# Kernel tuning notes

Hardware: AMD Instinct MI355X
Metric: run time of the kernel (lower is better)

Reference implementation:

```python
import jax, jax.numpy as jnp
import numpy as np

B, C, H, W = 32, 64, 128, 128


def setup_inputs() -> dict:
    key = jax.random.key(0)
    ks = jax.random.split(key, 9)
    s = 1.0 / np.sqrt(C)
    return {
        "q": jax.random.normal(ks[0], (B, C, H, W), dtype=jnp.float32),
        "k": jax.random.normal(ks[1], (B, C, H, W), dtype=jnp.float32),
        "v": jax.random.normal(ks[2], (B, C, H, W), dtype=jnp.float32),
        "wq": jax.random.normal(ks[3], (C, C), dtype=jnp.float32) * s,
        "bq": jax.random.normal(ks[4], (C,), dtype=jnp.float32) * s,
        "wk": jax.random.normal(ks[5], (C, C), dtype=jnp.float32) * s,
        "bk": jax.random.normal(ks[6], (C,), dtype=jnp.float32) * s,
        "wv": jax.random.normal(ks[7], (C, C), dtype=jnp.float32) * s,
        "bv": jax.random.normal(ks[8], (C,), dtype=jnp.float32) * s,
    }


def reference(q, k, v, wq, bq, wk, bk, wv, bv):
    # 1x1 conv == per-pixel linear over channels; fuse permute(0,2,3,1) into einsum
    qp = jnp.einsum('bchw,oc->bhwo', q, wq) + bq  # [B,H,W,C]
    kp = jnp.einsum('bchw,oc->bhwo', k, wk) + bk  # [B,H,W,C]
    vp = jnp.einsum('bchw,oc->bhwo', v, wv) + bv  # [B,H,W,C]
    # unnormalized attention along W axis, batched over (B, H)
    attn = jnp.einsum('bhwc,bhxc->bhwx', qp, kp)   # [B,H,W,W]
    out = jnp.einsum('bhwx,bhxc->bhwc', attn, vp)  # [B,H,W,C]
    return jnp.transpose(out, (0, 3, 1, 2)) + q    # back to [B,C,H,W] + residual
```

## Files before the change

### kernel.cpp

```cpp
#include <hip/hip_runtime.h>
#include <hip/hip_bf16.h>


typedef __bf16 bf16x8 __attribute__((ext_vector_type(8)));
typedef float  f32x4  __attribute__((ext_vector_type(4)));

#define LDP 68
#define LDX 132

#define OF_A 0
#define OF_B 8704
#define OF_C 17408
#define OF_D 25856
#define OF_W 34304
#define OF_SB 38656
#define LDS_USHORTS (38656 + 384)

__device__ __forceinline__ unsigned short f2bf(float x) {
  __hip_bfloat16 h = __float2bfloat16(x);
  return __builtin_bit_cast(unsigned short, h);
}
__device__ __forceinline__ float bf2f(unsigned short u) {
  unsigned int t = ((unsigned int)u) << 16;
  return __builtin_bit_cast(float, t);
}
__device__ __forceinline__ unsigned int pack2(float a, float b) {
  return (unsigned int)f2bf(a) | ((unsigned int)f2bf(b) << 16);
}
__device__ __forceinline__ bf16x8 cvt8(float4 a, float4 b) {
  union { unsigned int u[4]; bf16x8 v; } r;
  r.u[0] = pack2(a.x, a.y); r.u[1] = pack2(a.z, a.w);
  r.u[2] = pack2(b.x, b.y); r.u[3] = pack2(b.z, b.w);
  return r.v;
}
__device__ __forceinline__ bf16x8 ld8(const unsigned short* p) {
  uint2 lo = *reinterpret_cast<const uint2*>(p);
  uint2 hi = *reinterpret_cast<const uint2*>(p + 4);
  uint4 t;
  t.x = lo.x; t.y = lo.y; t.z = hi.x; t.w = hi.y;
  return __builtin_bit_cast(bf16x8, t);
}

__global__ __launch_bounds__(512, 4)
void fused_mha(const float* __restrict__ q, const float* __restrict__ k,
               const float* __restrict__ v,
               const float* __restrict__ wq, const float* __restrict__ bq,
               const float* __restrict__ wk, const float* __restrict__ bk,
               const float* __restrict__ wv, const float* __restrict__ bv,
               float* __restrict__ out)
{
  __shared__ __align__(16) unsigned short lds[LDS_USHORTS];
  unsigned short* sK   = lds + OF_A;
  unsigned short* sV   = lds + OF_B;
  unsigned short* sKPt = lds + OF_C;
  unsigned short* sVPt = lds + OF_D;
  unsigned short* sWq  = lds + OF_W;
  unsigned short* sTt  = lds + OF_A;
  unsigned short* sQ   = lds + OF_B;
  unsigned short* sQP  = lds + OF_C;
  float* sB = (float*)(lds + OF_SB);

  const int tid  = threadIdx.x;
  const int lane = tid & 63;
  const int ww   = tid >> 6;
  const int l15  = lane & 15;
  const int g    = lane >> 4;

  const int bh = blockIdx.x;
  const int bi = bh >> 7;
  const int hi = bh & 127;
  const size_t CS   = 128*128;
  const size_t base = (size_t)bi * (64*CS) + (size_t)hi * 128;

  const int sw0 = 4*(tid & 31);
  const int scA = 2*((tid >> 5) & 15);

  const int rt = ww & 3;
  const int cb = (ww >> 2) * 4;
  bf16x8 wkf[2], wvf[2];
  #pragma unroll
  for (int ks = 0; ks < 2; ++ks) {
    const float* pk = wk + (16*rt + l15)*64 + 8*g + 32*ks;
    const float* pv = wv + (16*rt + l15)*64 + 8*g + 32*ks;
    wkf[ks] = cvt8(*(const float4*)pk, *(const float4*)(pk+4));
    wvf[ks] = cvt8(*(const float4*)pv, *(const float4*)(pv+4));
  }
  float4 qreg[4];
  #pragma unroll
  for (int u = 0; u < 2; ++u) {
    int c = scA + 32*u;
    qreg[2*u+0] = *(const float4*)(q + base + (size_t)c    *CS + sw0);
    qreg[2*u+1] = *(const float4*)(q + base + (size_t)(c+1)*CS + sw0);
  }
  #pragma unroll
  for (int u = 0; u < 2; ++u) {
    int c = scA + 32*u;
    float4 ka = *(const float4*)(k + base + (size_t)c    *CS + sw0);
    float4 kb = *(const float4*)(k + base + (size_t)(c+1)*CS + sw0);
    float4 va = *(const float4*)(v + base + (size_t)c    *CS + sw0);
    float4 vb = *(const float4*)(v + base + (size_t)(c+1)*CS + sw0);
    const float* kaf = (const float*)&ka; const float* kbf = (const float*)&kb;
    const float* vaf = (const float*)&va; const float* vbf = (const float*)&vb;
    #pragma unroll
    for (int j = 0; j < 4; ++j) {
      *(unsigned int*)&sK[(sw0+j)*LDP + c] = pack2(kaf[j], kbf[j]);
      *(unsigned int*)&sV[(sw0+j)*LDP + c] = pack2(vaf[j], vbf[j]);
    }
  }
  {
    const int o  = tid >> 3;
    const int c0 = (tid & 7) * 8;
    float4 a = *(const float4*)(wq + o*64 + c0);
    float4 b = *(const float4*)(wq + o*64 + c0 + 4);
    unsigned short* p = &sWq[o*LDP + c0];
    ((uint2*)p)[0] = make_uint2(pack2(a.x,a.y), pack2(a.z,a.w));
    ((uint2*)p)[1] = make_uint2(pack2(b.x,b.y), pack2(b.z,b.w));
  }
  if (tid < 64)        sB[tid]       = bq[tid];
  else if (tid < 128)  sB[tid]       = bk[tid-64];
  else if (tid < 192)  sB[tid]       = bv[tid-128];
  __syncthreads();

  {
    f32x4 z = {0.f,0.f,0.f,0.f};
    f32x4 acck[4] = {z,z,z,z}, accv[4] = {z,z,z,z};
    #pragma unroll
    for (int ks = 0; ks < 2; ++ks) {
      #pragma unroll
      for (int cc = 0; cc < 4; ++cc) {
        bf16x8 bk8 = ld8(&sK[(16*(cb+cc) + l15)*LDP + 32*ks + 8*g]);
        bf16x8 bv8 = ld8(&sV[(16*(cb+cc) + l15)*LDP + 32*ks + 8*g]);
        acck[cc] = __builtin_amdgcn_mfma_f32_16x16x32_bf16(wkf[ks], bk8, acck[cc], 0, 0, 0);
        accv[cc] = __builtin_amdgcn_mfma_f32_16x16x32_bf16(wvf[ks], bv8, accv[cc], 0, 0, 0);
      }
    }
    #pragma unroll
    for (int cc = 0; cc < 4; ++cc) {
      int x = 16*(cb+cc) + l15;
      #pragma unroll
      for (int r = 0; r < 4; ++r) {
        int o = 16*rt + 4*g + r;
        sKPt[o*LDX + x] = f2bf(acck[cc][r] + sB[64 + o]);
        sVPt[o*LDX + x] = f2bf(accv[cc][r] + sB[128 + o]);
      }
    }
  }
  __syncthreads();

  {
    const int rt2 = ww >> 1;
    const int cb2 = (ww & 1) * 2;
    f32x4 z = {0.f,0.f,0.f,0.f};
    f32x4 acc[2] = {z,z};
    #pragma unroll
    for (int ks = 0; ks < 4; ++ks) {
      bf16x8 a = ld8(&sVPt[(16*rt2 + l15)*LDX + 32*ks + 8*g]);
      #pragma unroll
      for (int cc = 0; cc < 2; ++cc) {
        bf16x8 b = ld8(&sKPt[(16*(cb2+cc) + l15)*LDX + 32*ks + 8*g]);
        acc[cc] = __builtin_amdgcn_mfma_f32_16x16x32_bf16(a, b, acc[cc], 0, 0, 0);
      }
    }
    #pragma unroll
    for (int u = 0; u < 2; ++u) {
      int c = scA + 32*u;
      const float* qa = (const float*)&qreg[2*u];
      const float* qb = (const float*)&qreg[2*u+1];
      #pragma unroll
      for (int j = 0; j < 4; ++j)
        *(unsigned int*)&sQ[(sw0+j)*LDP + c] = pack2(qa[j], qb[j]);
    }
    #pragma unroll
    for (int cc = 0; cc < 2; ++cc) {
      int d = 16*(cb2+cc) + l15;
      #pragma unroll
      for (int r = 0; r < 4; ++r)
        sTt[(16*rt2 + 4*g + r)*LDP + d] = f2bf(acc[cc][r]);
    }
  }
  __syncthreads();

  {
    f32x4 z = {0.f,0.f,0.f,0.f};
    f32x4 acc[4] = {z,z,z,z};
    #pragma unroll
    for (int ks = 0; ks < 2; ++ks) {
      bf16x8 a = ld8(&sQ[(16*ww + l15)*LDP + 32*ks + 8*g]);
      #pragma unroll
      for (int ct = 0; ct < 4; ++ct) {
        bf16x8 b = ld8(&sWq[(16*ct + l15)*LDP + 32*ks + 8*g]);
        acc[ct] = __builtin_amdgcn_mfma_f32_16x16x32_bf16(a, b, acc[ct], 0, 0, 0);
      }
    }
    #pragma unroll
    for (int ct = 0; ct < 4; ++ct) {
      float bias = sB[16*ct + l15];
      #pragma unroll
      for (int r = 0; r < 4; ++r)
        sQP[(16*ww + 4*g + r)*LDP + 16*ct + l15] = f2bf(acc[ct][r] + bias);
    }
  }
  __syncthreads();

  {
    f32x4 z = {0.f,0.f,0.f,0.f};
    f32x4 acc[4] = {z,z,z,z};
    #pragma unroll
    for (int ks = 0; ks < 2; ++ks) {
      bf16x8 a = ld8(&sQP[(16*ww + l15)*LDP + 32*ks + 8*g]);
      #pragma unroll
      for (int ct = 0; ct < 4; ++ct) {
        bf16x8 b = ld8(&sTt[(16*ct + l15)*LDP + 32*ks + 8*g]);
        acc[ct] = __builtin_amdgcn_mfma_f32_16x16x32_bf16(a, b, acc[ct], 0, 0, 0);
      }
    }
    #pragma unroll
    for (int ct = 0; ct < 4; ++ct) {
      int c  = 16*ct + l15;
      int w0 = 16*ww + 4*g;
      float4 o4;
      o4.x = acc[ct][0] + bf2f(sQ[(w0+0)*LDP + c]);
      o4.y = acc[ct][1] + bf2f(sQ[(w0+1)*LDP + c]);
      o4.z = acc[ct][2] + bf2f(sQ[(w0+2)*LDP + c]);
      o4.w = acc[ct][3] + bf2f(sQ[(w0+3)*LDP + c]);
      *reinterpret_cast<float4*>(out + base + (size_t)c * CS + w0) = o4;
    }
  }
}

extern "C" void kernel_launch(void* const* d_in, const int* in_sizes, int n_in,
                              void* d_out, int out_size, void* d_ws, size_t ws_size,
                              hipStream_t stream) {
  (void)in_sizes; (void)n_in; (void)d_ws; (void)ws_size; (void)out_size;
  const float* q  = (const float*)d_in[0];
  const float* k  = (const float*)d_in[1];
  const float* v  = (const float*)d_in[2];
  const float* wq = (const float*)d_in[3];
  const float* bq = (const float*)d_in[4];
  const float* wk = (const float*)d_in[5];
  const float* bk = (const float*)d_in[6];
  const float* wv = (const float*)d_in[7];
  const float* bv = (const float*)d_in[8];
  float* out = (float*)d_out;
  fused_mha<<<dim3(32*128), dim3(512), 0, stream>>>(q, k, v, wq, bq, wk, bk, wv, bv, out);
}
```

Baseline: 112.6 us.

## Make blocks loop over eight rows with register prefetch and swizzled LDS

Each block now processes eight consecutive (batch,row) slices in a loop instead of one, prefetching the next slice's q/k/v into registers while the current slice's matmuls run. An XOR swizzle is applied to the sK/sV/sQ LDS tiles to reduce bank conflicts on the transposed stores, and one intra-wave barrier is removed. The grid shrinks to 512 blocks, which lowers resident waves per CU and relies on the software prefetch to hide global-memory latency.

```diff
diff --git a/kernel.cpp b/kernel.cpp
--- a/kernel.cpp
+++ b/kernel.cpp
@@ -15,6 +15,8 @@
 #define OF_W 34304
 #define OF_SB 38656
 #define LDS_USHORTS (38656 + 384)
+
+#define SWZ(row, col) ((col) ^ ((((row) >> 2) & 7) << 3))
 
 __device__ __forceinline__ unsigned short f2bf(float x) {
   __hip_bfloat16 h = __float2bfloat16(x);
@@ -66,14 +68,11 @@
   const int l15  = lane & 15;
   const int g    = lane >> 4;
 
-  const int bh = blockIdx.x;
-  const int bi = bh >> 7;
-  const int hi = bh & 127;
-  const size_t CS   = 128*128;
-  const size_t base = (size_t)bi * (64*CS) + (size_t)hi * 128;
-
-  const int sw0 = 4*(tid & 31);
-  const int scA = 2*((tid >> 5) & 15);
+  const size_t CS = 128*128;
+
+  const int sw0   = 4*(tid & 31);
+  const int scA   = 2*((tid >> 5) & 15);
+  const int swsel = ((tid & 31) & 7) << 3;
 
   const int rt = ww & 3;
   const int cb = (ww >> 2) * 4;
@@ -85,28 +84,6 @@
     wkf[ks] = cvt8(*(const float4*)pk, *(const float4*)(pk+4));
     wvf[ks] = cvt8(*(const float4*)pv, *(const float4*)(pv+4));
   }
-  float4 qreg[4];
-  #pragma unroll
-  for (int u = 0; u < 2; ++u) {
-    int c = scA + 32*u;
-    qreg[2*u+0] = *(const float4*)(q + base + (size_t)c    *CS + sw0);
-    qreg[2*u+1] = *(const float4*)(q + base + (size_t)(c+1)*CS + sw0);
-  }
-  #pragma unroll
-  for (int u = 0; u < 2; ++u) {
-    int c = scA + 32*u;
-    float4 ka = *(const float4*)(k + base + (size_t)c    *CS + sw0);
-    float4 kb = *(const float4*)(k + base + (size_t)(c+1)*CS + sw0);
-    float4 va = *(const float4*)(v + base + (size_t)c    *CS + sw0);
-    float4 vb = *(const float4*)(v + base + (size_t)(c+1)*CS + sw0);
-    const float* kaf = (const float*)&ka; const float* kbf = (const float*)&kb;
-    const float* vaf = (const float*)&va; const float* vbf = (const float*)&vb;
-    #pragma unroll
-    for (int j = 0; j < 4; ++j) {
-      *(unsigned int*)&sK[(sw0+j)*LDP + c] = pack2(kaf[j], kbf[j]);
-      *(unsigned int*)&sV[(sw0+j)*LDP + c] = pack2(vaf[j], vbf[j]);
-    }
-  }
   {
     const int o  = tid >> 3;
     const int c0 = (tid & 7) * 8;
@@ -116,115 +93,176 @@
     ((uint2*)p)[0] = make_uint2(pack2(a.x,a.y), pack2(a.z,a.w));
     ((uint2*)p)[1] = make_uint2(pack2(b.x,b.y), pack2(b.z,b.w));
   }
-  if (tid < 64)        sB[tid]       = bq[tid];
-  else if (tid < 128)  sB[tid]       = bk[tid-64];
-  else if (tid < 192)  sB[tid]       = bv[tid-128];
-  __syncthreads();
-
+  if (tid < 64)        sB[tid] = bq[tid];
+  else if (tid < 128)  sB[tid] = bk[tid-64];
+  else if (tid < 192)  sB[tid] = bv[tid-128];
+
+  float4 qreg[4], kreg[4], vreg[4];
   {
-    f32x4 z = {0.f,0.f,0.f,0.f};
-    f32x4 acck[4] = {z,z,z,z}, accv[4] = {z,z,z,z};
-    #pragma unroll
-    for (int ks = 0; ks < 2; ++ks) {
-      #pragma unroll
-      for (int cc = 0; cc < 4; ++cc) {
-        bf16x8 bk8 = ld8(&sK[(16*(cb+cc) + l15)*LDP + 32*ks + 8*g]);
-        bf16x8 bv8 = ld8(&sV[(16*(cb+cc) + l15)*LDP + 32*ks + 8*g]);
-        acck[cc] = __builtin_amdgcn_mfma_f32_16x16x32_bf16(wkf[ks], bk8, acck[cc], 0, 0, 0);
-        accv[cc] = __builtin_amdgcn_mfma_f32_16x16x32_bf16(wvf[ks], bv8, accv[cc], 0, 0, 0);
-      }
-    }
-    #pragma unroll
-    for (int cc = 0; cc < 4; ++cc) {
-      int x = 16*(cb+cc) + l15;
-      #pragma unroll
-      for (int r = 0; r < 4; ++r) {
-        int o = 16*rt + 4*g + r;
-        sKPt[o*LDX + x] = f2bf(acck[cc][r] + sB[64 + o]);
-        sVPt[o*LDX + x] = f2bf(accv[cc][r] + sB[128 + o]);
-      }
-    }
-  }
-  __syncthreads();
-
-  {
-    const int rt2 = ww >> 1;
-    const int cb2 = (ww & 1) * 2;
-    f32x4 z = {0.f,0.f,0.f,0.f};
-    f32x4 acc[2] = {z,z};
-    #pragma unroll
-    for (int ks = 0; ks < 4; ++ks) {
-      bf16x8 a = ld8(&sVPt[(16*rt2 + l15)*LDX + 32*ks + 8*g]);
-      #pragma unroll
-      for (int cc = 0; cc < 2; ++cc) {
-        bf16x8 b = ld8(&sKPt[(16*(cb2+cc) + l15)*LDX + 32*ks + 8*g]);
-        acc[cc] = __builtin_amdgcn_mfma_f32_16x16x32_bf16(a, b, acc[cc], 0, 0, 0);
-      }
-    }
+    const int bh = blockIdx.x << 3;
+    const size_t b0 = (size_t)(bh >> 7)*(64*CS) + (size_t)(bh & 127)*128;
     #pragma unroll
     for (int u = 0; u < 2; ++u) {
       int c = scA + 32*u;
-      const float* qa = (const float*)&qreg[2*u];
-      const float* qb = (const float*)&qreg[2*u+1];
-      #pragma unroll
-      for (int j = 0; j < 4; ++j)
-        *(unsigned int*)&sQ[(sw0+j)*LDP + c] = pack2(qa[j], qb[j]);
-    }
+      const float* pq = q + b0 + (size_t)c*CS + sw0;
+      const float* pk = k + b0 + (size_t)c*CS + sw0;
+      const float* pv = v + b0 + (size_t)c*CS + sw0;
+      qreg[2*u+0] = *(const float4*)pq;  qreg[2*u+1] = *(const float4*)(pq + CS);
+      kreg[2*u+0] = *(const float4*)pk;  kreg[2*u+1] = *(const float4*)(pk + CS);
+      vreg[2*u+0] = *(const float4*)pv;  vreg[2*u+1] = *(const float4*)(pv + CS);
+    }
+  }
+
+  for (int t = 0; t < 8; ++t) {
+    const int bh = (blockIdx.x << 3) + t;
+    const size_t base = (size_t)(bh >> 7)*(64*CS) + (size_t)(bh & 127)*128;
+    size_t nbase = 0;
+    if (t < 7) {
+      const int nbh = bh + 1;
+      nbase = (size_t)(nbh >> 7)*(64*CS) + (size_t)(nbh & 127)*128;
+    }
+
     #pragma unroll
-    for (int cc = 0; cc < 2; ++cc) {
-      int d = 16*(cb2+cc) + l15;
-      #pragma unroll
-      for (int r = 0; r < 4; ++r)
-        sTt[(16*rt2 + 4*g + r)*LDP + d] = f2bf(acc[cc][r]);
-    }
-  }
-  __syncthreads();
-
-  {
-    f32x4 z = {0.f,0.f,0.f,0.f};
-    f32x4 acc[4] = {z,z,z,z};
-    #pragma unroll
-    for (int ks = 0; ks < 2; ++ks) {
-      bf16x8 a = ld8(&sQ[(16*ww + l15)*LDP + 32*ks + 8*g]);
+    for (int u = 0; u < 2; ++u) {
+      int c = (scA + 32*u) ^ swsel;
+      const float* ka = (const float*)&kreg[2*u];
+      const float* kb = (const float*)&kreg[2*u+1];
+      const float* va = (const float*)&vreg[2*u];
+      const float* vb = (const float*)&vreg[2*u+1];
+      #pragma unroll
+      for (int j = 0; j < 4; ++j) {
+        *(unsigned int*)&sK[(sw0+j)*LDP + c] = pack2(ka[j], kb[j]);
+        *(unsigned int*)&sV[(sw0+j)*LDP + c] = pack2(va[j], vb[j]);
+      }
+    }
+    __syncthreads();
+
+    {
+      f32x4 z = {0.f,0.f,0.f,0.f};
+      f32x4 acck[4] = {z,z,z,z}, accv[4] = {z,z,z,z};
+      #pragma unroll
+      for (int ks = 0; ks < 2; ++ks) {
+        #pragma unroll
+        for (int cc = 0; cc < 4; ++cc) {
+          int row = 16*(cb+cc) + l15;
+          int col = SWZ(row, 32*ks + 8*g);
+          bf16x8 bk8 = ld8(&sK[row*LDP + col]);
+          bf16x8 bv8 = ld8(&sV[row*LDP + col]);
+          acck[cc] = __builtin_amdgcn_mfma_f32_16x16x32_bf16(wkf[ks], bk8, acck[cc], 0, 0, 0);
+          accv[cc] = __builtin_amdgcn_mfma_f32_16x16x32_bf16(wvf[ks], bv8, accv[cc], 0, 0, 0);
+        }
+      }
+      #pragma unroll
+      for (int cc = 0; cc < 4; ++cc) {
+        int x = 16*(cb+cc) + l15;
+        #pragma unroll
+        for (int r = 0; r < 4; ++r) {
+          int o = 16*rt + 4*g + r;
+          sKPt[o*LDX + x] = f2bf(acck[cc][r] + sB[64 + o]);
+          sVPt[o*LDX + x] = f2bf(accv[cc][r] + sB[128 + o]);
+        }
+      }
+    }
+    __syncthreads();
+
+    if (t < 7) {
+      #pragma unroll
+      for (int u = 0; u < 2; ++u) {
+        int c = scA + 32*u;
+        const float* pk = k + nbase + (size_t)c*CS + sw0;
+        const float* pv = v + nbase + (size_t)c*CS + sw0;
+        kreg[2*u+0] = *(const float4*)pk;  kreg[2*u+1] = *(const float4*)(pk + CS);
+        vreg[2*u+0] = *(const float4*)pv;  vreg[2*u+1] = *(const float4*)(pv + CS);
+      }
+    }
+    {
+      const int rt2 = ww >> 1;
+      const int cb2 = (ww & 1) * 2;
+      f32x4 z = {0.f,0.f,0.f,0.f};
+      f32x4 acc[2] = {z,z};
+      #pragma unroll
+      for (int ks = 0; ks < 4; ++ks) {
+        bf16x8 a = ld8(&sVPt[(16*rt2 + l15)*LDX + 32*ks + 8*g]);
+        #pragma unroll
+        for (int cc = 0; cc < 2; ++cc) {
+          bf16x8 b = ld8(&sKPt[(16*(cb2+cc) + l15)*LDX + 32*ks + 8*g]);
+          acc[cc] = __builtin_amdgcn_mfma_f32_16x16x32_bf16(a, b, acc[cc], 0, 0, 0);
+        }
+      }
+      #pragma unroll
+      for (int u = 0; u < 2; ++u) {
+        int c = (scA + 32*u) ^ swsel;
+        const float* qa = (const float*)&qreg[2*u];
+        const float* qb = (const float*)&qreg[2*u+1];
+        #pragma unroll
+        for (int j = 0; j < 4; ++j)
+          *(unsigned int*)&sQ[(sw0+j)*LDP + c] = pack2(qa[j], qb[j]);
+      }
+      #pragma unroll
+      for (int cc = 0; cc < 2; ++cc) {
+        int d = 16*(cb2+cc) + l15;
+        #pragma unroll
+        for (int r = 0; r < 4; ++r)
+          sTt[(16*rt2 + 4*g + r)*LDP + d] = f2bf(acc[cc][r]);
+      }
+    }
+    __syncthreads();
+
+    if (t < 7) {
+      #pragma unroll
+      for (int u = 0; u < 2; ++u) {
+        int c = scA + 32*u;
+        const float* pq = q + nbase + (size_t)c*CS + sw0;
+        qreg[2*u+0] = *(const float4*)pq;  qreg[2*u+1] = *(const float4*)(pq + CS);
+      }
+    }
+    {
+      f32x4 z = {0.f,0.f,0.f,0.f};
+      f32x4 acc[4] = {z,z,z,z};
+      #pragma unroll
+      for (int ks = 0; ks < 2; ++ks) {
+        int row = 16*ww + l15;
+        bf16x8 a = ld8(&sQ[row*LDP + SWZ(row, 32*ks + 8*g)]);
+        #pragma unroll
+        for (int ct = 0; ct < 4; ++ct) {
+          bf16x8 b = ld8(&sWq[(16*ct + l15)*LDP + 32*ks + 8*g]);
+          acc[ct] = __builtin_amdgcn_mfma_f32_16x16x32_bf16(a, b, acc[ct], 0, 0, 0);
+        }
+      }
       #pragma unroll
       for (int ct = 0; ct < 4; ++ct) {
-        bf16x8 b = ld8(&sWq[(16*ct + l15)*LDP + 32*ks + 8*g]);
-        acc[ct] = __builtin_amdgcn_mfma_f32_16x16x32_bf16(a, b, acc[ct], 0, 0, 0);
-      }
-    }
-    #pragma unroll
-    for (int ct = 0; ct < 4; ++ct) {
-      float bias = sB[16*ct + l15];
-      #pragma unroll
-      for (int r = 0; r < 4; ++r)
-        sQP[(16*ww + 4*g + r)*LDP + 16*ct + l15] = f2bf(acc[ct][r] + bias);
-    }
-  }
-  __syncthreads();
-
-  {
-    f32x4 z = {0.f,0.f,0.f,0.f};
-    f32x4 acc[4] = {z,z,z,z};
-    #pragma unroll
-    for (int ks = 0; ks < 2; ++ks) {
-      bf16x8 a = ld8(&sQP[(16*ww + l15)*LDP + 32*ks + 8*g]);
+        float bias = sB[16*ct + l15];
+        #pragma unroll
+        for (int r = 0; r < 4; ++r)
+          sQP[(16*ww + 4*g + r)*LDP + 16*ct + l15] = f2bf(acc[ct][r] + bias);
+      }
+    }
+
+    {
+      f32x4 z = {0.f,0.f,0.f,0.f};
+      f32x4 acc[4] = {z,z,z,z};
+      #pragma unroll
+      for (int ks = 0; ks < 2; ++ks) {
+        bf16x8 a = ld8(&sQP[(16*ww + l15)*LDP + 32*ks + 8*g]);
+        #pragma unroll
+        for (int ct = 0; ct < 4; ++ct) {
+          bf16x8 b = ld8(&sTt[(16*ct + l15)*LDP + 32*ks + 8*g]);
+          acc[ct] = __builtin_amdgcn_mfma_f32_16x16x32_bf16(a, b, acc[ct], 0, 0, 0);
+        }
+      }
       #pragma unroll
       for (int ct = 0; ct < 4; ++ct) {
-        bf16x8 b = ld8(&sTt[(16*ct + l15)*LDP + 32*ks + 8*g]);
-        acc[ct] = __builtin_amdgcn_mfma_f32_16x16x32_bf16(a, b, acc[ct], 0, 0, 0);
-      }
-    }
-    #pragma unroll
-    for (int ct = 0; ct < 4; ++ct) {
-      int c  = 16*ct + l15;
-      int w0 = 16*ww + 4*g;
-      float4 o4;
-      o4.x = acc[ct][0] + bf2f(sQ[(w0+0)*LDP + c]);
-      o4.y = acc[ct][1] + bf2f(sQ[(w0+1)*LDP + c]);
-      o4.z = acc[ct][2] + bf2f(sQ[(w0+2)*LDP + c]);
-      o4.w = acc[ct][3] + bf2f(sQ[(w0+3)*LDP + c]);
-      *reinterpret_cast<float4*>(out + base + (size_t)c * CS + w0) = o4;
-    }
+        int c  = 16*ct + l15;
+        int w0 = 16*ww + 4*g;
+        float4 o4;
+        o4.x = acc[ct][0] + bf2f(sQ[(w0+0)*LDP + SWZ(w0+0, c)]);
+        o4.y = acc[ct][1] + bf2f(sQ[(w0+1)*LDP + SWZ(w0+1, c)]);
+        o4.z = acc[ct][2] + bf2f(sQ[(w0+2)*LDP + SWZ(w0+2, c)]);
+        o4.w = acc[ct][3] + bf2f(sQ[(w0+3)*LDP + SWZ(w0+3, c)]);
+        *reinterpret_cast<float4*>(out + base + (size_t)c * CS + w0) = o4;
+      }
+    }
+    __syncthreads();
   }
 }
 
@@ -242,5 +280,5 @@
   const float* wv = (const float*)d_in[7];
   const float* bv = (const float*)d_in[8];
   float* out = (float*)d_out;
-  fused_mha<<<dim3(32*128), dim3(512), 0, stream>>>(q, k, v, wq, bq, wk, bk, wv, bv, out);
-}
+  fused_mha<<<dim3(512), dim3(512), 0, stream>>>(q, k, v, wq, bq, wk, bk, wv, bv, out);
+}
```

Result: slower. 173.3 us (+53.8%).

## Halve LDS footprint by processing K/V projection in two W-halves with swizzled layout

Applied to the files above, without the earlier changes.

The K/V projection and the V^T·K product now run over two 64-column halves of the W axis, reusing half-sized LDS staging buffers. The LDS budget per block drops substantially, which should let more blocks reside per CU, and the launch-bounds hint is raised to match. An XOR swizzle is applied to the staged K/V/Q tiles to reduce bank conflicts on the transposed writes. One barrier between the Q-projection and output stages is removed because each wave only reads back its own rows. The costs are an extra barrier per half and more serialized phases, and the Q loads move later in the kernel.

```diff
diff --git a/kernel.cpp b/kernel.cpp
--- a/kernel.cpp
+++ b/kernel.cpp
@@ -6,15 +6,17 @@
 typedef float  f32x4  __attribute__((ext_vector_type(4)));
 
 #define LDP 68
-#define LDX 132
-
-#define OF_A 0
-#define OF_B 8704
-#define OF_C 17408
-#define OF_D 25856
-#define OF_W 34304
-#define OF_SB 38656
-#define LDS_USHORTS (38656 + 384)
+
+#define OF_KS 0
+#define OF_VS 4352
+#define OF_KP 8704
+#define OF_VP 13056
+#define OF_TT 17408
+#define OF_WQ 21760
+#define OF_SB 26112
+#define LDS_USHORTS (26112 + 384)
+
+#define SWZ(row, col) ((col) ^ ((((row) >> 2) & 7) << 3))
 
 __device__ __forceinline__ unsigned short f2bf(float x) {
   __hip_bfloat16 h = __float2bfloat16(x);
@@ -41,7 +43,7 @@
   return __builtin_bit_cast(bf16x8, t);
 }
 
-__global__ __launch_bounds__(512, 4)
+__global__ __launch_bounds__(512, 6)
 void fused_mha(const float* __restrict__ q, const float* __restrict__ k,
                const float* __restrict__ v,
                const float* __restrict__ wq, const float* __restrict__ bq,
@@ -50,14 +52,14 @@
                float* __restrict__ out)
 {
   __shared__ __align__(16) unsigned short lds[LDS_USHORTS];
-  unsigned short* sK   = lds + OF_A;
-  unsigned short* sV   = lds + OF_B;
-  unsigned short* sKPt = lds + OF_C;
-  unsigned short* sVPt = lds + OF_D;
-  unsigned short* sWq  = lds + OF_W;
-  unsigned short* sTt  = lds + OF_A;
-  unsigned short* sQ   = lds + OF_B;
-  unsigned short* sQP  = lds + OF_C;
+  unsigned short* sKS = lds + OF_KS;
+  unsigned short* sVS = lds + OF_VS;
+  unsigned short* sKP = lds + OF_KP;
+  unsigned short* sVP = lds + OF_VP;
+  unsigned short* sTt = lds + OF_TT;
+  unsigned short* sWq = lds + OF_WQ;
+  unsigned short* sQ  = lds + OF_KS;
+  unsigned short* sQP = lds + OF_KP;
   float* sB = (float*)(lds + OF_SB);
 
   const int tid  = threadIdx.x;
@@ -66,17 +68,24 @@
   const int l15  = lane & 15;
   const int g    = lane >> 4;
 
+  const size_t CS = 128*128;
   const int bh = blockIdx.x;
-  const int bi = bh >> 7;
-  const int hi = bh & 127;
-  const size_t CS   = 128*128;
-  const size_t base = (size_t)bi * (64*CS) + (size_t)hi * 128;
-
-  const int sw0 = 4*(tid & 31);
-  const int scA = 2*((tid >> 5) & 15);
-
+  const size_t base = (size_t)(bh >> 7)*(64*CS) + (size_t)(bh & 127)*128;
+
+  const int sw0 = 4*(tid & 15);
+  const int scA = 2*((tid >> 4) & 31);
+  const int swk = ((tid & 15) & 7) << 3;
+
+  float4 kreg[4], vreg[4];
+  #pragma unroll
+  for (int h = 0; h < 2; ++h)
+    #pragma unroll
+    for (int e = 0; e < 2; ++e) {
+      kreg[2*h+e] = *(const float4*)(k + base + (size_t)(scA+e)*CS + sw0 + 64*h);
+      vreg[2*h+e] = *(const float4*)(v + base + (size_t)(scA+e)*CS + sw0 + 64*h);
+    }
   const int rt = ww & 3;
-  const int cb = (ww >> 2) * 4;
+  const int xb = (ww >> 2) * 2;
   bf16x8 wkf[2], wvf[2];
   #pragma unroll
   for (int ks = 0; ks < 2; ++ks) {
@@ -85,28 +94,6 @@
     wkf[ks] = cvt8(*(const float4*)pk, *(const float4*)(pk+4));
     wvf[ks] = cvt8(*(const float4*)pv, *(const float4*)(pv+4));
   }
-  float4 qreg[4];
-  #pragma unroll
-  for (int u = 0; u < 2; ++u) {
-    int c = scA + 32*u;
-    qreg[2*u+0] = *(const float4*)(q + base + (size_t)c    *CS + sw0);
-    qreg[2*u+1] = *(const float4*)(q + base + (size_t)(c+1)*CS + sw0);
-  }
-  #pragma unroll
-  for (int u = 0; u < 2; ++u) {
-    int c = scA + 32*u;
-    float4 ka = *(const float4*)(k + base + (size_t)c    *CS + sw0);
-    float4 kb = *(const float4*)(k + base + (size_t)(c+1)*CS + sw0);
-    float4 va = *(const float4*)(v + base + (size_t)c    *CS + sw0);
-    float4 vb = *(const float4*)(v + base + (size_t)(c+1)*CS + sw0);
-    const float* kaf = (const float*)&ka; const float* kbf = (const float*)&kb;
-    const float* vaf = (const float*)&va; const float* vbf = (const float*)&vb;
-    #pragma unroll
-    for (int j = 0; j < 4; ++j) {
-      *(unsigned int*)&sK[(sw0+j)*LDP + c] = pack2(kaf[j], kbf[j]);
-      *(unsigned int*)&sV[(sw0+j)*LDP + c] = pack2(vaf[j], vbf[j]);
-    }
-  }
   {
     const int o  = tid >> 3;
     const int c0 = (tid & 7) * 8;
@@ -116,76 +103,117 @@
     ((uint2*)p)[0] = make_uint2(pack2(a.x,a.y), pack2(a.z,a.w));
     ((uint2*)p)[1] = make_uint2(pack2(b.x,b.y), pack2(b.z,b.w));
   }
-  if (tid < 64)        sB[tid]       = bq[tid];
-  else if (tid < 128)  sB[tid]       = bk[tid-64];
-  else if (tid < 192)  sB[tid]       = bv[tid-128];
+  if (tid < 64)        sB[tid] = bq[tid];
+  else if (tid < 128)  sB[tid] = bk[tid-64];
+  else if (tid < 192)  sB[tid] = bv[tid-128];
+
+  {
+    const int c = scA ^ swk;
+    const float* ka = (const float*)&kreg[0];
+    const float* kb = (const float*)&kreg[1];
+    const float* va = (const float*)&vreg[0];
+    const float* vb = (const float*)&vreg[1];
+    #pragma unroll
+    for (int j = 0; j < 4; ++j) {
+      *(unsigned int*)&sKS[(sw0+j)*LDP + c] = pack2(ka[j], kb[j]);
+      *(unsigned int*)&sVS[(sw0+j)*LDP + c] = pack2(va[j], vb[j]);
+    }
+  }
   __syncthreads();
 
-  {
-    f32x4 z = {0.f,0.f,0.f,0.f};
-    f32x4 acck[4] = {z,z,z,z}, accv[4] = {z,z,z,z};
+  f32x4 z = {0.f,0.f,0.f,0.f};
+  f32x4 tacc[2] = {z, z};
+  const int rt2 = ww >> 1;
+  const int cb2 = (ww & 1) * 2;
+  float4 qreg[4];
+
+  #pragma unroll
+  for (int h = 0; h < 2; ++h) {
+    {
+      f32x4 acck[2] = {z,z}, accv[2] = {z,z};
+      #pragma unroll
+      for (int ks = 0; ks < 2; ++ks) {
+        #pragma unroll
+        for (int cc = 0; cc < 2; ++cc) {
+          int row = 16*(xb+cc) + l15;
+          int col = SWZ(row, 32*ks + 8*g);
+          bf16x8 bk8 = ld8(&sKS[row*LDP + col]);
+          bf16x8 bv8 = ld8(&sVS[row*LDP + col]);
+          acck[cc] = __builtin_amdgcn_mfma_f32_16x16x32_bf16(wkf[ks], bk8, acck[cc], 0, 0, 0);
+          accv[cc] = __builtin_amdgcn_mfma_f32_16x16x32_bf16(wvf[ks], bv8, accv[cc], 0, 0, 0);
+        }
+      }
+      #pragma unroll
+      for (int cc = 0; cc < 2; ++cc) {
+        int xl = 16*(xb+cc) + l15;
+        #pragma unroll
+        for (int r = 0; r < 4; ++r) {
+          int o = 16*rt + 4*g + r;
+          sKP[o*LDP + xl] = f2bf(acck[cc][r] + sB[64 + o]);
+          sVP[o*LDP + xl] = f2bf(accv[cc][r] + sB[128 + o]);
+        }
+      }
+    }
+    __syncthreads();
+
+    if (h == 0) {
+      const int c = scA ^ swk;
+      const float* ka = (const float*)&kreg[2];
+      const float* kb = (const float*)&kreg[3];
+      const float* va = (const float*)&vreg[2];
+      const float* vb = (const float*)&vreg[3];
+      #pragma unroll
+      for (int j = 0; j < 4; ++j) {
+        *(unsigned int*)&sKS[(sw0+j)*LDP + c] = pack2(ka[j], kb[j]);
+        *(unsigned int*)&sVS[(sw0+j)*LDP + c] = pack2(va[j], vb[j]);
+      }
+      #pragma unroll
+      for (int hh = 0; hh < 2; ++hh)
+        #pragma unroll
+        for (int e = 0; e < 2; ++e)
+          qreg[2*hh+e] = *(const float4*)(q + base + (size_t)(scA+e)*CS + sw0 + 64*hh);
+    } else {
+      #pragma unroll
+      for (int hh = 0; hh < 2; ++hh) {
+        const int c = scA ^ swk;
+        const float* qa = (const float*)&qreg[2*hh];
+        const float* qb = (const float*)&qreg[2*hh+1];
+        #pragma unroll
+        for (int j = 0; j < 4; ++j)
+          *(unsigned int*)&sQ[(sw0 + 64*hh + j)*LDP + c] = pack2(qa[j], qb[j]);
+      }
+    }
+    {
+      #pragma unroll
+      for (int ks = 0; ks < 2; ++ks) {
+        int arow = 16*rt2 + l15;
+        bf16x8 a = ld8(&sVP[arow*LDP + 32*ks + 8*g]);
+        #pragma unroll
+        for (int cc = 0; cc < 2; ++cc) {
+          int brow = 16*(cb2+cc) + l15;
+          bf16x8 b = ld8(&sKP[brow*LDP + 32*ks + 8*g]);
+          tacc[cc] = __builtin_amdgcn_mfma_f32_16x16x32_bf16(a, b, tacc[cc], 0, 0, 0);
+        }
+      }
+    }
+    if (h == 1) {
+      #pragma unroll
+      for (int cc = 0; cc < 2; ++cc) {
+        int d = 16*(cb2+cc) + l15;
+        #pragma unroll
+        for (int r = 0; r < 4; ++r)
+          sTt[(16*rt2 + 4*g + r)*LDP + d] = f2bf(tacc[cc][r]);
+      }
+    }
+    __syncthreads();
+  }
+
+  {
+    f32x4 acc[4] = {z,z,z,z};
     #pragma unroll
     for (int ks = 0; ks < 2; ++ks) {
-      #pragma unroll
-      for (int cc = 0; cc < 4; ++cc) {
-        bf16x8 bk8 = ld8(&sK[(16*(cb+cc) + l15)*LDP + 32*ks + 8*g]);
-        bf16x8 bv8 = ld8(&sV[(16*(cb+cc) + l15)*LDP + 32*ks + 8*g]);
-        acck[cc] = __builtin_amdgcn_mfma_f32_16x16x32_bf16(wkf[ks], bk8, acck[cc], 0, 0, 0);
-        accv[cc] = __builtin_amdgcn_mfma_f32_16x16x32_bf16(wvf[ks], bv8, accv[cc], 0, 0, 0);
-      }
-    }
-    #pragma unroll
-    for (int cc = 0; cc < 4; ++cc) {
-      int x = 16*(cb+cc) + l15;
-      #pragma unroll
-      for (int r = 0; r < 4; ++r) {
-        int o = 16*rt + 4*g + r;
-        sKPt[o*LDX + x] = f2bf(acck[cc][r] + sB[64 + o]);
-        sVPt[o*LDX + x] = f2bf(accv[cc][r] + sB[128 + o]);
-      }
-    }
-  }
-  __syncthreads();
-
-  {
-    const int rt2 = ww >> 1;
-    const int cb2 = (ww & 1) * 2;
-    f32x4 z = {0.f,0.f,0.f,0.f};
-    f32x4 acc[2] = {z,z};
-    #pragma unroll
-    for (int ks = 0; ks < 4; ++ks) {
-      bf16x8 a = ld8(&sVPt[(16*rt2 + l15)*LDX + 32*ks + 8*g]);
-      #pragma unroll
-      for (int cc = 0; cc < 2; ++cc) {
-        bf16x8 b = ld8(&sKPt[(16*(cb2+cc) + l15)*LDX + 32*ks + 8*g]);
-        acc[cc] = __builtin_amdgcn_mfma_f32_16x16x32_bf16(a, b, acc[cc], 0, 0, 0);
-      }
-    }
-    #pragma unroll
-    for (int u = 0; u < 2; ++u) {
-      int c = scA + 32*u;
-      const float* qa = (const float*)&qreg[2*u];
-      const float* qb = (const float*)&qreg[2*u+1];
-      #pragma unroll
-      for (int j = 0; j < 4; ++j)
-        *(unsigned int*)&sQ[(sw0+j)*LDP + c] = pack2(qa[j], qb[j]);
-    }
-    #pragma unroll
-    for (int cc = 0; cc < 2; ++cc) {
-      int d = 16*(cb2+cc) + l15;
-      #pragma unroll
-      for (int r = 0; r < 4; ++r)
-        sTt[(16*rt2 + 4*g + r)*LDP + d] = f2bf(acc[cc][r]);
-    }
-  }
-  __syncthreads();
-
-  {
-    f32x4 z = {0.f,0.f,0.f,0.f};
-    f32x4 acc[4] = {z,z,z,z};
-    #pragma unroll
-    for (int ks = 0; ks < 2; ++ks) {
-      bf16x8 a = ld8(&sQ[(16*ww + l15)*LDP + 32*ks + 8*g]);
+      int arow = 16*ww + l15;
+      bf16x8 a = ld8(&sQ[arow*LDP + SWZ(arow, 32*ks + 8*g)]);
       #pragma unroll
       for (int ct = 0; ct < 4; ++ct) {
         bf16x8 b = ld8(&sWq[(16*ct + l15)*LDP + 32*ks + 8*g]);
@@ -200,10 +228,8 @@
         sQP[(16*ww + 4*g + r)*LDP + 16*ct + l15] = f2bf(acc[ct][r] + bias);
     }
   }
-  __syncthreads();
-
-  {
-    f32x4 z = {0.f,0.f,0.f,0.f};
+
+  {
     f32x4 acc[4] = {z,z,z,z};
     #pragma unroll
     for (int ks = 0; ks < 2; ++ks) {
@@ -219,10 +245,10 @@
       int c  = 16*ct + l15;
       int w0 = 16*ww + 4*g;
       float4 o4;
-      o4.x = acc[ct][0] + bf2f(sQ[(w0+0)*LDP + c]);
-      o4.y = acc[ct][1] + bf2f(sQ[(w0+1)*LDP + c]);
-      o4.z = acc[ct][2] + bf2f(sQ[(w0+2)*LDP + c]);
-      o4.w = acc[ct][3] + bf2f(sQ[(w0+3)*LDP + c]);
+      o4.x = acc[ct][0] + bf2f(sQ[(w0+0)*LDP + SWZ(w0+0, c)]);
+      o4.y = acc[ct][1] + bf2f(sQ[(w0+1)*LDP + SWZ(w0+1, c)]);
+      o4.z = acc[ct][2] + bf2f(sQ[(w0+2)*LDP + SWZ(w0+2, c)]);
+      o4.w = acc[ct][3] + bf2f(sQ[(w0+3)*LDP + SWZ(w0+3, c)]);
       *reinterpret_cast<float4*>(out + base + (size_t)c * CS + w0) = o4;
     }
   }
```

After: 148.2 us. +31.6%, slower.
